# Kernel tuning notes

Hardware: AMD Instinct MI355X
Metric: run time of the kernel (lower is better)

Reference implementation:

```python
import jax, jax.numpy as jnp
import numpy as np

# Build the three 3x3x3 Sobel kernels once, stacked as [O=3, I=1, 3,3,3]
def _sobel_kernels():
    kx = np.array([[[-1,0,1],[-2,0,2],[-1,0,1]],
                   [[-2,0,2],[-4,0,4],[-2,0,2]],
                   [[-1,0,1],[-2,0,2],[-1,0,1]]], dtype=np.float32)
    ky = np.array([[[-1,-2,-1],[0,0,0],[1,2,1]],
                   [[-2,-4,-2],[0,0,0],[2,4,2]],
                   [[-1,-2,-1],[0,0,0],[1,2,1]]], dtype=np.float32)
    kz = np.array([[[-1,-2,-1],[-2,-4,-2],[-1,-2,-1]],
                   [[0,0,0],[0,0,0],[0,0,0]],
                   [[1,2,1],[2,4,2],[1,2,1]]], dtype=np.float32)
    return jnp.asarray(np.stack([kx, ky, kz])[:, None])  # [3,1,3,3,3]

_K = _sobel_kernels()
_EPS = 1e-08

def _grad_mag(x):
    # x: [B,1,D,H,W] -> fused conv producing all 3 gradient channels at once
    g = jax.lax.conv_general_dilated(
        x, _K, window_strides=(1, 1, 1), padding='SAME',
        dimension_numbers=('NCDHW', 'OIDHW', 'NCDHW'))  # [B,3,D,H,W]
    return jnp.sqrt(jnp.sum(g * g, axis=1, keepdims=True) + _EPS)  # [B,1,D,H,W]


def setup_inputs() -> dict:
    key = jax.random.key(0)
    k1, k2 = jax.random.split(key)
    shape = (2, 1, 160, 192, 160)
    pred = jax.random.normal(k1, shape, dtype=jnp.float32)
    target = jax.random.normal(k2, shape, dtype=jnp.float32)
    return {"pred": pred, "target": target}


def reference(pred, target):
    pg = _grad_mag(pred)
    tg = _grad_mag(target)
    # penalty='l1' -> F.l1_loss mean reduction
    return jnp.mean(jnp.abs(pg - tg))
```

## Files before the change

kernel.cpp:

```cpp
#include <hip/hip_runtime.h>

namespace {
constexpr int Wd = 160, Hd = 192, Dd = 160, Bd = 2;
constexpr int HW = Hd * Wd;
constexpr int THREADS = 256;
constexpr int ROWS_OUT = 6;
constexpr int ROWS_LDS = 8;
constexpr int RS = 164;
constexpr int STRIPS = 40;
constexpr int CTHREADS = ROWS_OUT * STRIPS;
constexpr int TASKS = 2 * ROWS_LDS * STRIPS;
constexpr int DCHUNK = 10;
constexpr int NCHUNK = Dd / DCHUNK;
constexpr int RGROUPS = Hd / ROWS_OUT;
constexpr float EPS = 1e-8f;
}

using v4f = __attribute__((ext_vector_type(4))) float;
using v4h = __attribute__((ext_vector_type(4))) _Float16;

__device__ __forceinline__ float dpp_up1(float v) {
  return __int_as_float(__builtin_amdgcn_update_dpp(
      0, __float_as_int(v), 0x138, 0xF, 0xF, true));
}
__device__ __forceinline__ float dpp_dn1(float v) {
  return __int_as_float(__builtin_amdgcn_update_dpp(
      0, __float_as_int(v), 0x130, 0xF, 0xF, true));
}

__global__ __launch_bounds__(THREADS) void sobel_loss_kernel(
    const float* __restrict__ pred, const float* __restrict__ targ,
    float* __restrict__ out) {
  __shared__ __align__(16) _Float16 lsw[2][ROWS_LDS][RS];
  __shared__ __align__(16) _Float16 ldw[2][ROWS_LDS][RS];
  const int tid = threadIdx.x;
  const int lane = tid & 63;
  const int h0 = blockIdx.x * ROWS_OUT;
  const int d0 = blockIdx.y * DCHUNK;
  const size_t volOff = (size_t)blockIdx.z * Dd * HW;
  const float* pb = pred + volOff;
  const float* tb = targ + volOff;

  const float* gs[3];
  _Float16* psw[3];
  _Float16* pdw[3];
  bool sok[3], rok[3], zL[3], zR[3], pL[3], pR[3];
#pragma unroll
  for (int u = 0; u < 3; ++u) {
    const int i = tid + 256 * u;
    const bool ok = (i < TASKS);
    const int ic = ok ? i : 0;
    const int t_ = ic / (ROWS_LDS * STRIPS);
    const int rem = ic - t_ * (ROWS_LDS * STRIPS);
    const int r8 = rem / STRIPS, s = rem - r8 * STRIPS;
    const int hh = h0 - 1 + r8;
    const bool rv = ok && ((unsigned)hh < (unsigned)Hd);
    sok[u] = ok;
    rok[u] = rv;
    zL[u] = (s == 0);
    zR[u] = (s == STRIPS - 1);
    pL[u] = ok && (lane == 0) && (s != 0);
    pR[u] = ok && (lane == 63) && (s != STRIPS - 1);
    gs[u] = (t_ ? tb : pb) + (size_t)(rv ? hh : 0) * Wd + s * 4;
    psw[u] = &lsw[t_][r8][s * 4];
    pdw[u] = &ldw[t_][r8][s * 4];
  }

  float4 m[3];
  float hl[3], hr[3];
  auto GLOAD = [&](int d) {
    const bool dok = (unsigned)d < (unsigned)Dd;
    const size_t so = (size_t)d * HW;
#pragma unroll
    for (int u = 0; u < 3; ++u) {
      float4 v = make_float4(0.f, 0.f, 0.f, 0.f);
      float a = 0.f, b = 0.f;
      if (dok && rok[u]) {
        v = *reinterpret_cast<const float4*>(gs[u] + so);
        if (pL[u]) a = gs[u][so - 1];
        if (pR[u]) b = gs[u][so + 4];
      }
      m[u] = v; hl[u] = a; hr[u] = b;
    }
  };

  auto STAGE = [&]() {
#pragma unroll
    for (int u = 0; u < 3; ++u) {
      float xl = dpp_up1(m[u].w);
      float xr = dpp_dn1(m[u].x);
      if (zL[u]) xl = 0.f;
      if (pL[u]) xl = hl[u];
      if (zR[u]) xr = 0.f;
      if (pR[u]) xr = hr[u];
      const float x0 = xl, x1 = m[u].x, x2 = m[u].y, x3 = m[u].z,
                  x4 = m[u].w, x5 = xr;
      v4f swf, dwf;
      swf[0] = fmaf(2.f, x1, x0 + x2);  dwf[0] = x2 - x0;
      swf[1] = fmaf(2.f, x2, x1 + x3);  dwf[1] = x3 - x1;
      swf[2] = fmaf(2.f, x3, x2 + x4);  dwf[2] = x4 - x2;
      swf[3] = fmaf(2.f, x4, x3 + x5);  dwf[3] = x5 - x3;
      if (sok[u]) {
        *reinterpret_cast<v4h*>(psw[u]) = __builtin_convertvector(swf, v4h);
        *reinterpret_cast<v4h*>(pdw[u]) = __builtin_convertvector(dwf, v4h);
      }
    }
  };

  const int cr = tid / STRIPS;
  const int cs4 = (tid - cr * STRIPS) * 4;
  const bool is_c = (tid < CTHREADS);

  v4h A[3][2], B[3][2], C[3][2];
  const _Float16 h2 = (_Float16)2.0f;

  auto HCONV = [&](int slot) {
#pragma unroll
    for (int t_ = 0; t_ < 2; ++t_) {
      const v4h sm = *reinterpret_cast<const v4h*>(&lsw[t_][cr][cs4]);
      const v4h s0 = *reinterpret_cast<const v4h*>(&lsw[t_][cr + 1][cs4]);
      const v4h sp = *reinterpret_cast<const v4h*>(&lsw[t_][cr + 2][cs4]);
      const v4h dm = *reinterpret_cast<const v4h*>(&ldw[t_][cr][cs4]);
      const v4h dd = *reinterpret_cast<const v4h*>(&ldw[t_][cr + 1][cs4]);
      const v4h dp = *reinterpret_cast<const v4h*>(&ldw[t_][cr + 2][cs4]);
      A[slot][t_] = s0 * h2 + (sm + sp);
      B[slot][t_] = dd * h2 + (dm + dp);
      C[slot][t_] = sp - sm;
    }
  };

  v4f accv = {0.f, 0.f, 0.f, 0.f};

  GLOAD(d0 - 1);
  STAGE(); GLOAD(d0); __syncthreads();
  if (is_c) HCONV(0);
  __syncthreads();
  STAGE(); GLOAD(d0 + 1); __syncthreads();
  if (is_c) HCONV(1);
  __syncthreads();

#pragma unroll
  for (int k = 0; k < DCHUNK; ++k) {
    STAGE();
    if (k < DCHUNK - 1) GLOAD(d0 + 2 + k);
    __syncthreads();
    const int i0 = k % 3, i1 = (k + 1) % 3, i2 = (k + 2) % 3;
    if (is_c) {
      HCONV(i2);
      const v4h gx0 = B[i1][0] * h2 + (B[i0][0] + B[i2][0]);
      const v4h gy0 = C[i1][0] * h2 + (C[i0][0] + C[i2][0]);
      const v4h gz0 = A[i2][0] - A[i0][0];
      const v4h q0h = gx0 * gx0 + gy0 * gy0 + gz0 * gz0;
      const v4h gx1 = B[i1][1] * h2 + (B[i0][1] + B[i2][1]);
      const v4h gy1 = C[i1][1] * h2 + (C[i0][1] + C[i2][1]);
      const v4h gz1 = A[i2][1] - A[i0][1];
      const v4h q1h = gx1 * gx1 + gy1 * gy1 + gz1 * gz1;
      const v4f q0 = __builtin_convertvector(q0h, v4f) + EPS;
      const v4f q1 = __builtin_convertvector(q1h, v4f) + EPS;
      v4f dd_;
#pragma unroll
      for (int j = 0; j < 4; ++j)
        dd_[j] = __builtin_amdgcn_sqrtf(q0[j]) - __builtin_amdgcn_sqrtf(q1[j]);
#pragma unroll
      for (int j = 0; j < 4; ++j) dd_[j] = fabsf(dd_[j]);
      accv += dd_;
    }
    __syncthreads();
  }

  float sred = accv[0] + accv[1] + accv[2] + accv[3];
#pragma unroll
  for (int off = 32; off > 0; off >>= 1) sred += __shfl_down(sred, off, 64);
  __shared__ float wsum[THREADS / 64];
  const int wid = tid >> 6;
  if (lane == 0) wsum[wid] = sred;
  __syncthreads();
  if (tid == 0) {
    float t = 0.f;
#pragma unroll
    for (int i = 0; i < THREADS / 64; ++i) t += wsum[i];
    atomicAdd(out, t * (1.0f / (float)((size_t)Bd * Dd * Hd * Wd)));
  }
}

extern "C" void kernel_launch(void* const* d_in, const int* in_sizes, int n_in,
                              void* d_out, int out_size, void* d_ws, size_t ws_size,
                              hipStream_t stream) {
  const float* pred = (const float*)d_in[0];
  const float* targ = (const float*)d_in[1];
  float* out = (float*)d_out;
  (void)in_sizes; (void)n_in; (void)out_size; (void)d_ws; (void)ws_size;

  hipMemsetAsync(out, 0, sizeof(float), stream);
  dim3 grid(RGROUPS, NCHUNK, Bd);
  sobel_loss_kernel<<<grid, THREADS, 0, stream>>>(pred, targ, out);
}
```

Before: 35.53 us.

## Factor vertical Sobel smoothing into pairwise row sums in LDS staging

Staging threads now each load up to four adjacent rows and write pairwise sums of consecutive rows (7 pairs instead of 8 raw rows) into LDS. The [1,2,1] H-filter is factored as [1,1]*[1,1], so HCONV reads two LDS rows instead of three and does fewer half-precision ops. The cost is a changed thread-to-work mapping: staging threads load more rows each (4 vs up to 3), and the per-thread work is uneven because some groups handle 3 rows and others 4. Summing pairs in fp32 before converting to fp16 also shifts the rounding slightly.

```diff
diff --git a/kernel.cpp b/kernel.cpp
--- a/kernel.cpp
+++ b/kernel.cpp
@@ -5,11 +5,11 @@
 constexpr int HW = Hd * Wd;
 constexpr int THREADS = 256;
 constexpr int ROWS_OUT = 6;
-constexpr int ROWS_LDS = 8;
+constexpr int PAIRS = 7;
 constexpr int RS = 164;
 constexpr int STRIPS = 40;
 constexpr int CTHREADS = ROWS_OUT * STRIPS;
-constexpr int TASKS = 2 * ROWS_LDS * STRIPS;
+constexpr int STHREADS = 240;
 constexpr int DCHUNK = 10;
 constexpr int NCHUNK = Dd / DCHUNK;
 constexpr int RGROUPS = Hd / ROWS_OUT;
@@ -31,8 +31,8 @@
 __global__ __launch_bounds__(THREADS) void sobel_loss_kernel(
     const float* __restrict__ pred, const float* __restrict__ targ,
     float* __restrict__ out) {
-  __shared__ __align__(16) _Float16 lsw[2][ROWS_LDS][RS];
-  __shared__ __align__(16) _Float16 ldw[2][ROWS_LDS][RS];
+  __shared__ __align__(16) _Float16 lps[2][PAIRS][RS];
+  __shared__ __align__(16) _Float16 lpd[2][PAIRS][RS];
   const int tid = threadIdx.x;
   const int lane = tid & 63;
   const int h0 = blockIdx.x * ROWS_OUT;
@@ -41,68 +41,81 @@
   const float* pb = pred + volOff;
   const float* tb = targ + volOff;
 
-  const float* gs[3];
-  _Float16* psw[3];
-  _Float16* pdw[3];
-  bool sok[3], rok[3], zL[3], zR[3], pL[3], pR[3];
-#pragma unroll
-  for (int u = 0; u < 3; ++u) {
-    const int i = tid + 256 * u;
-    const bool ok = (i < TASKS);
-    const int ic = ok ? i : 0;
-    const int t_ = ic / (ROWS_LDS * STRIPS);
-    const int rem = ic - t_ * (ROWS_LDS * STRIPS);
-    const int r8 = rem / STRIPS, s = rem - r8 * STRIPS;
-    const int hh = h0 - 1 + r8;
-    const bool rv = ok && ((unsigned)hh < (unsigned)Hd);
-    sok[u] = ok;
-    rok[u] = rv;
-    zL[u] = (s == 0);
-    zR[u] = (s == STRIPS - 1);
-    pL[u] = ok && (lane == 0) && (s != 0);
-    pR[u] = ok && (lane == 63) && (s != STRIPS - 1);
-    gs[u] = (t_ ? tb : pb) + (size_t)(rv ? hh : 0) * Wd + s * 4;
-    psw[u] = &lsw[t_][r8][s * 4];
-    pdw[u] = &ldw[t_][r8][s * 4];
-  }
-
-  float4 m[3];
-  float hl[3], hr[3];
+  const int g = tid / 80;
+  const int q = tid - g * 80;
+  const int t_ = q / 40;
+  const int s = q - t_ * 40;
+  const bool is_s = (tid < STHREADS);
+  const int r0 = 2 * g;
+  const int nr = (g < 2) ? 3 : 4;
+  const int np = (g < 2) ? 2 : 3;
+
+  const float* gsj[4];
+  bool rvj[4];
+#pragma unroll
+  for (int j = 0; j < 4; ++j) {
+    const int hh = h0 - 1 + r0 + j;
+    const bool jn = is_s && (j < nr);
+    rvj[j] = jn && ((unsigned)hh < (unsigned)Hd);
+    gsj[j] = (t_ ? tb : pb) + (size_t)(rvj[j] ? hh : 0) * Wd + s * 4;
+  }
+  const bool zL = (s == 0), zR = (s == STRIPS - 1);
+  const bool pL = is_s && (lane == 0) && !zL;
+  const bool pR = is_s && (lane == 63) && !zR;
+
+  _Float16* pps[3];
+  _Float16* ppd[3];
+  bool pok[3];
+#pragma unroll
+  for (int p = 0; p < 3; ++p) {
+    pok[p] = is_s && (p < np);
+    const int pr = pok[p] ? (r0 + p) : 0;
+    pps[p] = &lps[t_][pr][s * 4];
+    ppd[p] = &lpd[t_][pr][s * 4];
+  }
+
+  float4 m[4];
+  float hl[4], hr[4];
   auto GLOAD = [&](int d) {
     const bool dok = (unsigned)d < (unsigned)Dd;
     const size_t so = (size_t)d * HW;
 #pragma unroll
-    for (int u = 0; u < 3; ++u) {
+    for (int j = 0; j < 4; ++j) {
       float4 v = make_float4(0.f, 0.f, 0.f, 0.f);
       float a = 0.f, b = 0.f;
-      if (dok && rok[u]) {
-        v = *reinterpret_cast<const float4*>(gs[u] + so);
-        if (pL[u]) a = gs[u][so - 1];
-        if (pR[u]) b = gs[u][so + 4];
+      if (dok && rvj[j]) {
+        v = *reinterpret_cast<const float4*>(gsj[j] + so);
+        if (pL) a = gsj[j][so - 1];
+        if (pR) b = gsj[j][so + 4];
       }
-      m[u] = v; hl[u] = a; hr[u] = b;
+      m[j] = v; hl[j] = a; hr[j] = b;
     }
   };
 
   auto STAGE = [&]() {
-#pragma unroll
-    for (int u = 0; u < 3; ++u) {
-      float xl = dpp_up1(m[u].w);
-      float xr = dpp_dn1(m[u].x);
-      if (zL[u]) xl = 0.f;
-      if (pL[u]) xl = hl[u];
-      if (zR[u]) xr = 0.f;
-      if (pR[u]) xr = hr[u];
-      const float x0 = xl, x1 = m[u].x, x2 = m[u].y, x3 = m[u].z,
-                  x4 = m[u].w, x5 = xr;
-      v4f swf, dwf;
-      swf[0] = fmaf(2.f, x1, x0 + x2);  dwf[0] = x2 - x0;
-      swf[1] = fmaf(2.f, x2, x1 + x3);  dwf[1] = x3 - x1;
-      swf[2] = fmaf(2.f, x3, x2 + x4);  dwf[2] = x4 - x2;
-      swf[3] = fmaf(2.f, x4, x3 + x5);  dwf[3] = x5 - x3;
-      if (sok[u]) {
-        *reinterpret_cast<v4h*>(psw[u]) = __builtin_convertvector(swf, v4h);
-        *reinterpret_cast<v4h*>(pdw[u]) = __builtin_convertvector(dwf, v4h);
+    v4f swf[4], dwf[4];
+#pragma unroll
+    for (int j = 0; j < 4; ++j) {
+      float xl = dpp_up1(m[j].w);
+      float xr = dpp_dn1(m[j].x);
+      if (zL) xl = 0.f;
+      if (pL) xl = hl[j];
+      if (zR) xr = 0.f;
+      if (pR) xr = hr[j];
+      const float x0 = xl, x1 = m[j].x, x2 = m[j].y, x3 = m[j].z,
+                  x4 = m[j].w, x5 = xr;
+      swf[j][0] = fmaf(2.f, x1, x0 + x2);  dwf[j][0] = x2 - x0;
+      swf[j][1] = fmaf(2.f, x2, x1 + x3);  dwf[j][1] = x3 - x1;
+      swf[j][2] = fmaf(2.f, x3, x2 + x4);  dwf[j][2] = x4 - x2;
+      swf[j][3] = fmaf(2.f, x4, x3 + x5);  dwf[j][3] = x5 - x3;
+    }
+#pragma unroll
+    for (int p = 0; p < 3; ++p) {
+      if (pok[p]) {
+        const v4f psv = swf[p] + swf[p + 1];
+        const v4f pdv = dwf[p] + dwf[p + 1];
+        *reinterpret_cast<v4h*>(pps[p]) = __builtin_convertvector(psv, v4h);
+        *reinterpret_cast<v4h*>(ppd[p]) = __builtin_convertvector(pdv, v4h);
       }
     }
   };
@@ -112,24 +125,22 @@
   const bool is_c = (tid < CTHREADS);
 
   v4h A[3][2], B[3][2], C[3][2];
+
+  auto HCONV = [&](int slot) {
+#pragma unroll
+    for (int tt = 0; tt < 2; ++tt) {
+      const v4h pa = *reinterpret_cast<const v4h*>(&lps[tt][cr][cs4]);
+      const v4h pb2 = *reinterpret_cast<const v4h*>(&lps[tt][cr + 1][cs4]);
+      const v4h da = *reinterpret_cast<const v4h*>(&lpd[tt][cr][cs4]);
+      const v4h db = *reinterpret_cast<const v4h*>(&lpd[tt][cr + 1][cs4]);
+      A[slot][tt] = pa + pb2;
+      B[slot][tt] = da + db;
+      C[slot][tt] = pb2 - pa;
+    }
+  };
+
+  v4f accv = {0.f, 0.f, 0.f, 0.f};
   const _Float16 h2 = (_Float16)2.0f;
-
-  auto HCONV = [&](int slot) {
-#pragma unroll
-    for (int t_ = 0; t_ < 2; ++t_) {
-      const v4h sm = *reinterpret_cast<const v4h*>(&lsw[t_][cr][cs4]);
-      const v4h s0 = *reinterpret_cast<const v4h*>(&lsw[t_][cr + 1][cs4]);
-      const v4h sp = *reinterpret_cast<const v4h*>(&lsw[t_][cr + 2][cs4]);
-      const v4h dm = *reinterpret_cast<const v4h*>(&ldw[t_][cr][cs4]);
-      const v4h dd = *reinterpret_cast<const v4h*>(&ldw[t_][cr + 1][cs4]);
-      const v4h dp = *reinterpret_cast<const v4h*>(&ldw[t_][cr + 2][cs4]);
-      A[slot][t_] = s0 * h2 + (sm + sp);
-      B[slot][t_] = dd * h2 + (dm + dp);
-      C[slot][t_] = sp - sm;
-    }
-  };
-
-  v4f accv = {0.f, 0.f, 0.f, 0.f};
 
   GLOAD(d0 - 1);
   STAGE(); GLOAD(d0); __syncthreads();
```

Result: slower. 38.52 us (+8.4%).

## Process two depth slices per barrier pair with double-buffered LDS staging

Applied to the files above, without the earlier changes.

Doubles the LDS staging buffers and register prefetch sets so each iteration stages, convolves and emits two depth slices between one pair of barriers instead of one. This halves the number of __syncthreads per chunk and puts two global loads in flight at a time. In exchange it doubles LDS use and raises register pressure, which could lower occupancy.

```diff
diff --git a/kernel.cpp b/kernel.cpp
--- a/kernel.cpp
+++ b/kernel.cpp
@@ -13,6 +13,7 @@
 constexpr int DCHUNK = 10;
 constexpr int NCHUNK = Dd / DCHUNK;
 constexpr int RGROUPS = Hd / ROWS_OUT;
+constexpr int BUFSTRIDE = 2 * ROWS_LDS * RS;
 constexpr float EPS = 1e-8f;
 }
 
@@ -31,8 +32,8 @@
 __global__ __launch_bounds__(THREADS) void sobel_loss_kernel(
     const float* __restrict__ pred, const float* __restrict__ targ,
     float* __restrict__ out) {
-  __shared__ __align__(16) _Float16 lsw[2][ROWS_LDS][RS];
-  __shared__ __align__(16) _Float16 ldw[2][ROWS_LDS][RS];
+  __shared__ __align__(16) _Float16 lsw[2][2][ROWS_LDS][RS];
+  __shared__ __align__(16) _Float16 ldw[2][2][ROWS_LDS][RS];
   const int tid = threadIdx.x;
   const int lane = tid & 63;
   const int h0 = blockIdx.x * ROWS_OUT;
@@ -62,13 +63,14 @@
     pL[u] = ok && (lane == 0) && (s != 0);
     pR[u] = ok && (lane == 63) && (s != STRIPS - 1);
     gs[u] = (t_ ? tb : pb) + (size_t)(rv ? hh : 0) * Wd + s * 4;
-    psw[u] = &lsw[t_][r8][s * 4];
-    pdw[u] = &ldw[t_][r8][s * 4];
+    psw[u] = &lsw[0][t_][r8][s * 4];
+    pdw[u] = &ldw[0][t_][r8][s * 4];
   }
 
-  float4 m[3];
-  float hl[3], hr[3];
-  auto GLOAD = [&](int d) {
+  float4 mA[3], mB[3];
+  float hlA[3], hrA[3], hlB[3], hrB[3];
+
+  auto GLOADto = [&](int d, float4 (&m)[3], float (&hl)[3], float (&hr)[3]) {
     const bool dok = (unsigned)d < (unsigned)Dd;
     const size_t so = (size_t)d * HW;
 #pragma unroll
@@ -84,7 +86,8 @@
     }
   };
 
-  auto STAGE = [&]() {
+  auto STAGEfrom = [&](int b, const float4 (&m)[3], const float (&hl)[3],
+                       const float (&hr)[3]) {
 #pragma unroll
     for (int u = 0; u < 3; ++u) {
       float xl = dpp_up1(m[u].w);
@@ -101,8 +104,10 @@
       swf[2] = fmaf(2.f, x3, x2 + x4);  dwf[2] = x4 - x2;
       swf[3] = fmaf(2.f, x4, x3 + x5);  dwf[3] = x5 - x3;
       if (sok[u]) {
-        *reinterpret_cast<v4h*>(psw[u]) = __builtin_convertvector(swf, v4h);
-        *reinterpret_cast<v4h*>(pdw[u]) = __builtin_convertvector(dwf, v4h);
+        *reinterpret_cast<v4h*>(psw[u] + b * BUFSTRIDE) =
+            __builtin_convertvector(swf, v4h);
+        *reinterpret_cast<v4h*>(pdw[u] + b * BUFSTRIDE) =
+            __builtin_convertvector(dwf, v4h);
       }
     }
   };
@@ -114,15 +119,15 @@
   v4h A[3][2], B[3][2], C[3][2];
   const _Float16 h2 = (_Float16)2.0f;
 
-  auto HCONV = [&](int slot) {
+  auto HCONV = [&](int slot, int b) {
 #pragma unroll
     for (int t_ = 0; t_ < 2; ++t_) {
-      const v4h sm = *reinterpret_cast<const v4h*>(&lsw[t_][cr][cs4]);
-      const v4h s0 = *reinterpret_cast<const v4h*>(&lsw[t_][cr + 1][cs4]);
-      const v4h sp = *reinterpret_cast<const v4h*>(&lsw[t_][cr + 2][cs4]);
-      const v4h dm = *reinterpret_cast<const v4h*>(&ldw[t_][cr][cs4]);
-      const v4h dd = *reinterpret_cast<const v4h*>(&ldw[t_][cr + 1][cs4]);
-      const v4h dp = *reinterpret_cast<const v4h*>(&ldw[t_][cr + 2][cs4]);
+      const v4h sm = *reinterpret_cast<const v4h*>(&lsw[b][t_][cr][cs4]);
+      const v4h s0 = *reinterpret_cast<const v4h*>(&lsw[b][t_][cr + 1][cs4]);
+      const v4h sp = *reinterpret_cast<const v4h*>(&lsw[b][t_][cr + 2][cs4]);
+      const v4h dm = *reinterpret_cast<const v4h*>(&ldw[b][t_][cr][cs4]);
+      const v4h dd = *reinterpret_cast<const v4h*>(&ldw[b][t_][cr + 1][cs4]);
+      const v4h dp = *reinterpret_cast<const v4h*>(&ldw[b][t_][cr + 2][cs4]);
       A[slot][t_] = s0 * h2 + (sm + sp);
       B[slot][t_] = dd * h2 + (dm + dp);
       C[slot][t_] = sp - sm;
@@ -131,39 +136,52 @@
 
   v4f accv = {0.f, 0.f, 0.f, 0.f};
 
-  GLOAD(d0 - 1);
-  STAGE(); GLOAD(d0); __syncthreads();
-  if (is_c) HCONV(0);
+  auto EMIT = [&](int i0, int i1, int i2) {
+    const v4h gx0 = B[i1][0] * h2 + (B[i0][0] + B[i2][0]);
+    const v4h gy0 = C[i1][0] * h2 + (C[i0][0] + C[i2][0]);
+    const v4h gz0 = A[i2][0] - A[i0][0];
+    const v4h q0h = gx0 * gx0 + gy0 * gy0 + gz0 * gz0;
+    const v4h gx1 = B[i1][1] * h2 + (B[i0][1] + B[i2][1]);
+    const v4h gy1 = C[i1][1] * h2 + (C[i0][1] + C[i2][1]);
+    const v4h gz1 = A[i2][1] - A[i0][1];
+    const v4h q1h = gx1 * gx1 + gy1 * gy1 + gz1 * gz1;
+    const v4f q0 = __builtin_convertvector(q0h, v4f) + EPS;
+    const v4f q1 = __builtin_convertvector(q1h, v4f) + EPS;
+    v4f dd_;
+#pragma unroll
+    for (int j = 0; j < 4; ++j)
+      dd_[j] = __builtin_amdgcn_sqrtf(q0[j]) - __builtin_amdgcn_sqrtf(q1[j]);
+#pragma unroll
+    for (int j = 0; j < 4; ++j) dd_[j] = fabsf(dd_[j]);
+    accv += dd_;
+  };
+
+  GLOADto(d0 - 1, mA, hlA, hrA);
+  GLOADto(d0,     mB, hlB, hrB);
+  STAGEfrom(0, mA, hlA, hrA);
+  STAGEfrom(1, mB, hlB, hrB);
+  GLOADto(d0 + 1, mA, hlA, hrA);
+  GLOADto(d0 + 2, mB, hlB, hrB);
   __syncthreads();
-  STAGE(); GLOAD(d0 + 1); __syncthreads();
-  if (is_c) HCONV(1);
+  if (is_c) { HCONV(0, 0); HCONV(1, 1); }
   __syncthreads();
 
 #pragma unroll
-  for (int k = 0; k < DCHUNK; ++k) {
-    STAGE();
-    if (k < DCHUNK - 1) GLOAD(d0 + 2 + k);
+  for (int j = 1; j <= DCHUNK / 2; ++j) {
+    STAGEfrom(0, mA, hlA, hrA);
+    STAGEfrom(1, mB, hlB, hrB);
+    if (j < DCHUNK / 2) {
+      GLOADto(d0 + 1 + 2 * j, mA, hlA, hrA);
+      GLOADto(d0 + 2 + 2 * j, mB, hlB, hrB);
+    }
     __syncthreads();
-    const int i0 = k % 3, i1 = (k + 1) % 3, i2 = (k + 2) % 3;
     if (is_c) {
-      HCONV(i2);
-      const v4h gx0 = B[i1][0] * h2 + (B[i0][0] + B[i2][0]);
-      const v4h gy0 = C[i1][0] * h2 + (C[i0][0] + C[i2][0]);
-      const v4h gz0 = A[i2][0] - A[i0][0];
-      const v4h q0h = gx0 * gx0 + gy0 * gy0 + gz0 * gz0;
-      const v4h gx1 = B[i1][1] * h2 + (B[i0][1] + B[i2][1]);
-      const v4h gy1 = C[i1][1] * h2 + (C[i0][1] + C[i2][1]);
-      const v4h gz1 = A[i2][1] - A[i0][1];
-      const v4h q1h = gx1 * gx1 + gy1 * gy1 + gz1 * gz1;
-      const v4f q0 = __builtin_convertvector(q0h, v4f) + EPS;
-      const v4f q1 = __builtin_convertvector(q1h, v4f) + EPS;
-      v4f dd_;
-#pragma unroll
-      for (int j = 0; j < 4; ++j)
-        dd_[j] = __builtin_amdgcn_sqrtf(q0[j]) - __builtin_amdgcn_sqrtf(q1[j]);
-#pragma unroll
-      for (int j = 0; j < 4; ++j) dd_[j] = fabsf(dd_[j]);
-      accv += dd_;
+      const int na = 2 * j;
+      HCONV(na % 3, 0);
+      EMIT((na + 1) % 3, (na + 2) % 3, na % 3);
+      const int nb = 2 * j + 1;
+      HCONV(nb % 3, 1);
+      EMIT((nb + 1) % 3, (nb + 2) % 3, nb % 3);
     }
     __syncthreads();
   }
```

Measured after the change: 35.75 us. No clear change (+0.6%).

## Double output rows per block, each compute thread handles two row halves

Applied to the files above, without the earlier changes.

Each block now produces 12 output rows instead of 6 and stages 14 halo rows in LDS. Every compute thread covers two rows 6 apart, and staging uses 5 load slots per thread. The cost being attacked is halo overhead: re-loading 2 halo rows per 6 outputs, with the repeated global loads and DPP/convert staging that go with them. In exchange the grid shrinks to half as many blocks, and per-thread register pressure rises from more in-flight loads and doubled A/B/C state, which could reduce occupancy.

```diff
diff --git a/kernel.cpp b/kernel.cpp
--- a/kernel.cpp
+++ b/kernel.cpp
@@ -4,12 +4,13 @@
 constexpr int Wd = 160, Hd = 192, Dd = 160, Bd = 2;
 constexpr int HW = Hd * Wd;
 constexpr int THREADS = 256;
-constexpr int ROWS_OUT = 6;
-constexpr int ROWS_LDS = 8;
+constexpr int ROWS_OUT = 12;
+constexpr int ROWS_LDS = 14;
 constexpr int RS = 164;
 constexpr int STRIPS = 40;
-constexpr int CTHREADS = ROWS_OUT * STRIPS;
+constexpr int CTHREADS = 240;
 constexpr int TASKS = 2 * ROWS_LDS * STRIPS;
+constexpr int NSLOT = 5;
 constexpr int DCHUNK = 10;
 constexpr int NCHUNK = Dd / DCHUNK;
 constexpr int RGROUPS = Hd / ROWS_OUT;
@@ -41,12 +42,12 @@
   const float* pb = pred + volOff;
   const float* tb = targ + volOff;
 
-  const float* gs[3];
-  _Float16* psw[3];
-  _Float16* pdw[3];
-  bool sok[3], rok[3], zL[3], zR[3], pL[3], pR[3];
-#pragma unroll
-  for (int u = 0; u < 3; ++u) {
+  const float* gs[NSLOT];
+  _Float16* psw[NSLOT];
+  _Float16* pdw[NSLOT];
+  bool sok[NSLOT], rok[NSLOT], zL[NSLOT], zR[NSLOT], pL[NSLOT], pR[NSLOT];
+#pragma unroll
+  for (int u = 0; u < NSLOT; ++u) {
     const int i = tid + 256 * u;
     const bool ok = (i < TASKS);
     const int ic = ok ? i : 0;
@@ -66,13 +67,13 @@
     pdw[u] = &ldw[t_][r8][s * 4];
   }
 
-  float4 m[3];
-  float hl[3], hr[3];
+  float4 m[NSLOT];
+  float hl[NSLOT], hr[NSLOT];
   auto GLOAD = [&](int d) {
     const bool dok = (unsigned)d < (unsigned)Dd;
     const size_t so = (size_t)d * HW;
 #pragma unroll
-    for (int u = 0; u < 3; ++u) {
+    for (int u = 0; u < NSLOT; ++u) {
       float4 v = make_float4(0.f, 0.f, 0.f, 0.f);
       float a = 0.f, b = 0.f;
       if (dok && rok[u]) {
@@ -86,7 +87,7 @@
 
   auto STAGE = [&]() {
 #pragma unroll
-    for (int u = 0; u < 3; ++u) {
+    for (int u = 0; u < NSLOT; ++u) {
       float xl = dpp_up1(m[u].w);
       float xr = dpp_dn1(m[u].x);
       if (zL[u]) xl = 0.f;
@@ -111,25 +112,52 @@
   const int cs4 = (tid - cr * STRIPS) * 4;
   const bool is_c = (tid < CTHREADS);
 
-  v4h A[3][2], B[3][2], C[3][2];
+  v4h A[3][2][2], B[3][2][2], C[3][2][2];
   const _Float16 h2 = (_Float16)2.0f;
 
   auto HCONV = [&](int slot) {
 #pragma unroll
-    for (int t_ = 0; t_ < 2; ++t_) {
-      const v4h sm = *reinterpret_cast<const v4h*>(&lsw[t_][cr][cs4]);
-      const v4h s0 = *reinterpret_cast<const v4h*>(&lsw[t_][cr + 1][cs4]);
-      const v4h sp = *reinterpret_cast<const v4h*>(&lsw[t_][cr + 2][cs4]);
-      const v4h dm = *reinterpret_cast<const v4h*>(&ldw[t_][cr][cs4]);
-      const v4h dd = *reinterpret_cast<const v4h*>(&ldw[t_][cr + 1][cs4]);
-      const v4h dp = *reinterpret_cast<const v4h*>(&ldw[t_][cr + 2][cs4]);
-      A[slot][t_] = s0 * h2 + (sm + sp);
-      B[slot][t_] = dd * h2 + (dm + dp);
-      C[slot][t_] = sp - sm;
+    for (int hf = 0; hf < 2; ++hf) {
+      const int r = cr + hf * 6;
+#pragma unroll
+      for (int t_ = 0; t_ < 2; ++t_) {
+        const v4h sm = *reinterpret_cast<const v4h*>(&lsw[t_][r][cs4]);
+        const v4h s0 = *reinterpret_cast<const v4h*>(&lsw[t_][r + 1][cs4]);
+        const v4h sp = *reinterpret_cast<const v4h*>(&lsw[t_][r + 2][cs4]);
+        const v4h dm = *reinterpret_cast<const v4h*>(&ldw[t_][r][cs4]);
+        const v4h dd = *reinterpret_cast<const v4h*>(&ldw[t_][r + 1][cs4]);
+        const v4h dp = *reinterpret_cast<const v4h*>(&ldw[t_][r + 2][cs4]);
+        A[slot][t_][hf] = s0 * h2 + (sm + sp);
+        B[slot][t_][hf] = dd * h2 + (dm + dp);
+        C[slot][t_][hf] = sp - sm;
+      }
     }
   };
 
   v4f accv = {0.f, 0.f, 0.f, 0.f};
+
+  auto EMITF = [&](int i0, int i1, int i2) {
+#pragma unroll
+    for (int hf = 0; hf < 2; ++hf) {
+      const v4h gx0 = B[i1][0][hf] * h2 + (B[i0][0][hf] + B[i2][0][hf]);
+      const v4h gy0 = C[i1][0][hf] * h2 + (C[i0][0][hf] + C[i2][0][hf]);
+      const v4h gz0 = A[i2][0][hf] - A[i0][0][hf];
+      const v4h q0h = gx0 * gx0 + gy0 * gy0 + gz0 * gz0;
+      const v4h gx1 = B[i1][1][hf] * h2 + (B[i0][1][hf] + B[i2][1][hf]);
+      const v4h gy1 = C[i1][1][hf] * h2 + (C[i0][1][hf] + C[i2][1][hf]);
+      const v4h gz1 = A[i2][1][hf] - A[i0][1][hf];
+      const v4h q1h = gx1 * gx1 + gy1 * gy1 + gz1 * gz1;
+      const v4f q0 = __builtin_convertvector(q0h, v4f) + EPS;
+      const v4f q1 = __builtin_convertvector(q1h, v4f) + EPS;
+      v4f dd_;
+#pragma unroll
+      for (int j = 0; j < 4; ++j)
+        dd_[j] = __builtin_amdgcn_sqrtf(q0[j]) - __builtin_amdgcn_sqrtf(q1[j]);
+#pragma unroll
+      for (int j = 0; j < 4; ++j) dd_[j] = fabsf(dd_[j]);
+      accv += dd_;
+    }
+  };
 
   GLOAD(d0 - 1);
   STAGE(); GLOAD(d0); __syncthreads();
@@ -147,23 +175,7 @@
     const int i0 = k % 3, i1 = (k + 1) % 3, i2 = (k + 2) % 3;
     if (is_c) {
       HCONV(i2);
-      const v4h gx0 = B[i1][0] * h2 + (B[i0][0] + B[i2][0]);
-      const v4h gy0 = C[i1][0] * h2 + (C[i0][0] + C[i2][0]);
-      const v4h gz0 = A[i2][0] - A[i0][0];
-      const v4h q0h = gx0 * gx0 + gy0 * gy0 + gz0 * gz0;
-      const v4h gx1 = B[i1][1] * h2 + (B[i0][1] + B[i2][1]);
-      const v4h gy1 = C[i1][1] * h2 + (C[i0][1] + C[i2][1]);
-      const v4h gz1 = A[i2][1] - A[i0][1];
-      const v4h q1h = gx1 * gx1 + gy1 * gy1 + gz1 * gz1;
-      const v4f q0 = __builtin_convertvector(q0h, v4f) + EPS;
-      const v4f q1 = __builtin_convertvector(q1h, v4f) + EPS;
-      v4f dd_;
-#pragma unroll
-      for (int j = 0; j < 4; ++j)
-        dd_[j] = __builtin_amdgcn_sqrtf(q0[j]) - __builtin_amdgcn_sqrtf(q1[j]);
-#pragma unroll
-      for (int j = 0; j < 4; ++j) dd_[j] = fabsf(dd_[j]);
-      accv += dd_;
+      EMITF(i0, i1, i2);
     }
     __syncthreads();
   }
```

New measurement: 33.84 us (median of 2 runs). 4.7% less time.
